# Kernel tuning notes

Hardware: AMD Instinct MI355X
Metric: run time of the kernel (lower is better)

## Reference

```python
import jax, jax.numpy as jnp
import numpy as np

ALPHA = 0.2          # LeakyReLU negative slope
NEG_INF = -9e15      # mask value used by the original module


def setup_inputs() -> dict:
    key = jax.random.key(0)
    k1, k2, k3, k4 = jax.random.split(key, 4)
    N, Din, Dout = 8192, 512, 256
    features = jax.random.normal(k1, (N, Din), dtype=jnp.float32)
    adj = jax.random.randint(k2, (N, N), 0, 2, dtype=jnp.int32)
    W = jax.random.normal(k3, (Din, Dout), dtype=jnp.float32) * (1.414 / np.sqrt(Din))
    a = jax.random.normal(k4, (2 * Dout, 1), dtype=jnp.float32) * (1.414 / np.sqrt(2 * Dout))
    return {"features": features, "adj": adj, "W": W, "a": a}


def reference(features, adj, W, a):
    Dout = W.shape[1]
    Wh = features @ W                       # [N, Dout]
    # e_ij = leakyrelu([Wh_i || Wh_j] @ a) decomposes additively:
    # identical math to the N*N*2D concat in the original, without materializing it.
    src = Wh @ a[:Dout, 0]                  # [N]  contribution of node i
    dst = Wh @ a[Dout:, 0]                  # [N]  contribution of node j
    e = jax.nn.leaky_relu(src[:, None] + dst[None, :], negative_slope=ALPHA)  # [N, N]
    masked = jnp.where(adj > 0, e, NEG_INF)
    attention = jax.nn.softmax(masked, axis=1)   # dropout p=0.0 (eval) -> identity
    h_prime = attention @ Wh                # [N, Dout]
    return jax.nn.elu(h_prime)
```

## Files before the change

kernel.cpp:

```cpp
#include <hip/hip_runtime.h>
#include <hip/hip_bf16.h>

#define NN   8192
#define DIN  512
#define DOUT 256

typedef __attribute__((ext_vector_type(8)))  short s16x8;
typedef __attribute__((ext_vector_type(16))) float f32x16;

static __device__ __forceinline__ unsigned short f2bf(float f) {
    union { float f; unsigned u; } v; v.f = f;
    unsigned r = v.u + 0x7fffu + ((v.u >> 16) & 1u);
    return (unsigned short)(r >> 16);
}

__global__ __launch_bounds__(256) void k_wh2(const float* __restrict__ feat,
                                             const float* __restrict__ W,
                                             const float* __restrict__ a,
                                             unsigned short* __restrict__ WhT,
                                             float* __restrict__ src,
                                             float* __restrict__ dst) {
    __shared__ float lf[16 * DIN];
    __shared__ float red[2][4][16];
    const int tid = threadIdx.x;
    const int i0  = blockIdx.x * 16;
    const int w   = tid >> 6, lane = tid & 63;

    const float4* fsrc = (const float4*)(feat + (size_t)i0 * DIN);
    float4* fdst = (float4*)lf;
    #pragma unroll
    for (int q = 0; q < 8; ++q) fdst[tid + q * 256] = fsrc[tid + q * 256];
    __syncthreads();

    const int c = tid;
    float outs[16];
    #pragma unroll
    for (int r = 0; r < 16; ++r) outs[r] = 0.f;

    for (int k = 0; k < DIN; k += 4) {
        float w0 = W[(k + 0) * DOUT + c];
        float w1 = W[(k + 1) * DOUT + c];
        float w2 = W[(k + 2) * DOUT + c];
        float w3 = W[(k + 3) * DOUT + c];
        #pragma unroll
        for (int r = 0; r < 16; ++r) {
            float4 f = *(const float4*)&lf[r * DIN + k];
            outs[r] = fmaf(f.x, w0, fmaf(f.y, w1, fmaf(f.z, w2, fmaf(f.w, w3, outs[r]))));
        }
    }

    unsigned short tb[16];
    #pragma unroll
    for (int r = 0; r < 16; ++r) tb[r] = f2bf(outs[r]);
    uint4* wt = (uint4*)(WhT + (size_t)c * NN + i0);
    wt[0] = *(uint4*)&tb[0];
    wt[1] = *(uint4*)&tb[8];

    const float as_ = a[c], ad_ = a[DOUT + c];
    #pragma unroll
    for (int r = 0; r < 16; ++r) {
        float s = outs[r] * as_;
        float d = outs[r] * ad_;
        #pragma unroll
        for (int off = 32; off; off >>= 1) {
            s += __shfl_xor(s, off);
            d += __shfl_xor(d, off);
        }
        if (lane == 0) { red[0][w][r] = s; red[1][w][r] = d; }
    }
    __syncthreads();
    if (tid < 16)
        src[i0 + tid] = red[0][0][tid] + red[0][1][tid] + red[0][2][tid] + red[0][3][tid];
    else if (tid < 32) {
        int r = tid - 16;
        dst[i0 + r] = red[1][0][r] + red[1][1][r] + red[1][2][r] + red[1][3][r];
    }
}

__global__ __launch_bounds__(256) void k_mask(const int* __restrict__ adj,
                                              unsigned char* __restrict__ bits) {
    const int row = blockIdx.x;
    const int tid = threadIdx.x;
    const int* base = adj + (size_t)row * NN + tid * 32;
    unsigned int u = 0;
    #pragma unroll
    for (int j = 0; j < 8; ++j) {
        int4 v = *(const int4*)(base + j * 4);
        unsigned int b = (v.x > 0 ? 1u : 0u) | (v.y > 0 ? 2u : 0u) |
                         (v.z > 0 ? 4u : 0u) | (v.w > 0 ? 8u : 0u);
        u |= b << (j * 4);
    }
    *(unsigned int*)(bits + (size_t)row * 1024 + tid * 4) = u;
}


#define STEP6(T, CUR)                                                                    \
{                                                                                        \
        \
    s16x8 bfr_[4];                                                                       \
    _Pragma("unroll")                                                                    \
    for (int ks4 = 0; ks4 < 4; ++ks4)                                                    \
        bfr_[ks4] = *(const s16x8*)(WhTb + (T) * 64 + ks4 * 16);                         \
                                       \
    if ((T) < 31) {                                                                      \
        const unsigned int m8_ = browp[((T) + 1) * 8];                                   \
        float4 d0_ = *(const float4*)(dstp + ((T) + 1) * 64);                            \
        float4 d1_ = *(const float4*)(dstp + ((T) + 1) * 64 + 4);                        \
        const float dd_[8] = {d0_.x, d0_.y, d0_.z, d0_.w, d1_.x, d1_.y, d1_.z, d1_.w};   \
        s16x8 pw_;                                                                       \
        _Pragma("unroll")                                                                \
        for (int jj = 0; jj < 8; ++jj) {                                                 \
            float x_ = si + dd_[jj];                                                     \
            x_ = fmaxf(x_, 0.2f * x_);                               \
            float p_ = (m8_ >> jj) & 1u ? __expf(x_) : 0.f;     \
            den += p_;                                                                   \
            pw_[jj] = (short)f2bf(p_);                                                   \
        }                                                                                \
        *(s16x8*)(Pl[(CUR) ^ 1] + pbyte) = pw_;                                          \
    }                                                                                    \
                             \
    _Pragma("unroll")                                                                    \
    for (int ks4 = 0; ks4 < 4; ++ks4) {                                                  \
        const int kbyte_ = ks4 * 32 + lhi * 16;                                          \
        _Pragma("unroll")                                                                \
        for (int mt = 0; mt < 2; ++mt) {                                                 \
            const int row_ = mt * 32 + l31;                                              \
            s16x8 afv_ = *(const s16x8*)(Pl[CUR] + row_ * 128 +                          \
                                         (kbyte_ ^ ((row_ & 7) << 4)));                  \
            acc[mt] = __builtin_amdgcn_mfma_f32_32x32x16_bf16(afv_, bfr_[ks4], acc[mt], 0, 0, 0); \
        }                                                                                \
    }                                                                                    \
    __syncthreads();                \
}

__global__ __launch_bounds__(512, 4) void k_attn6(const unsigned char* __restrict__ bits,
                                                  const unsigned short* __restrict__ WhT,
                                                  const float* __restrict__ src,
                                                  const float* __restrict__ dstg,
                                                  float* __restrict__ denp,
                                                  float* __restrict__ part) {
    __shared__ __attribute__((aligned(16))) char Pl[2][8192];

    const int tid  = threadIdx.x;
    const int lane = tid & 63;
    const int w    = tid >> 6;
    const int l31  = lane & 31, lhi = lane >> 5;
    const int c0w  = w * 32;

    const int rt  = blockIdx.x & 127;
    const int ks  = blockIdx.x >> 7;
    const int kb0 = ks * 2048;

    const unsigned short* WhTb = WhT + (size_t)(c0w + l31) * NN + kb0 + lhi * 8;

    const int r  = tid >> 3, kb = tid & 7;
    const int gr = rt * 64 + r;
    const float si = src[gr];
    const unsigned char* browp = bits + (size_t)gr * 1024 + ks * 256 + kb;
    const float* dstp = dstg + kb0 + kb * 8;
    const int pbyte = r * 128 + ((kb * 16) ^ ((r & 7) << 4));

    f32x16 acc[2];
    #pragma unroll
    for (int mt = 0; mt < 2; ++mt)
        #pragma unroll
        for (int e = 0; e < 16; ++e) acc[mt][e] = 0.f;
    float den = 0.f;

    {
        const unsigned int m8 = browp[0];
        float4 d0 = *(const float4*)(dstp);
        float4 d1 = *(const float4*)(dstp + 4);
        const float dd[8] = {d0.x, d0.y, d0.z, d0.w, d1.x, d1.y, d1.z, d1.w};
        s16x8 pw;
        #pragma unroll
        for (int jj = 0; jj < 8; ++jj) {
            float x = si + dd[jj];
            x = fmaxf(x, 0.2f * x);
            float p = (m8 >> jj) & 1u ? __expf(x) : 0.f;
            den += p;
            pw[jj] = (short)f2bf(p);
        }
        *(s16x8*)(Pl[0] + pbyte) = pw;
    }
    __syncthreads();

    for (int tt = 0; tt < 16; ++tt) {
        STEP6(2 * tt,     0);
        STEP6(2 * tt + 1, 1);
    }

    den += __shfl_xor(den, 1);
    den += __shfl_xor(den, 2);
    den += __shfl_xor(den, 4);
    if ((tid & 7) == 0) denp[(size_t)ks * NN + gr] = den;

    float* pp = part + (size_t)ks * (NN * DOUT);
    #pragma unroll
    for (int mt = 0; mt < 2; ++mt) {
        #pragma unroll
        for (int e = 0; e < 16; ++e) {
            const int row = rt * 64 + mt * 32 + (e & 3) + 8 * (e >> 2) + 4 * lhi;
            pp[(size_t)row * DOUT + c0w + l31] = acc[mt][e];
        }
    }
}

__global__ __launch_bounds__(256) void k_finish2(const float* __restrict__ part,
                                                 const float* __restrict__ denp,
                                                 float* __restrict__ out) {
    const int idx = blockIdx.x * 256 + threadIdx.x;
    const int row = idx >> 6;
    float den = denp[row] + denp[NN + row] + denp[2 * NN + row] + denp[3 * NN + row];
    float rv = den > 0.f ? 1.f / den : 0.f;
    const int st = NN * DOUT / 4;
    const float4* p = (const float4*)part;
    float4 va = p[idx], vb = p[idx + st], vc = p[idx + 2 * st], vd = p[idx + 3 * st];
    float4 s;
    s.x = (va.x + vb.x + vc.x + vd.x) * rv;
    s.y = (va.y + vb.y + vc.y + vd.y) * rv;
    s.z = (va.z + vb.z + vc.z + vd.z) * rv;
    s.w = (va.w + vb.w + vc.w + vd.w) * rv;
    s.x = s.x > 0.f ? s.x : expm1f(s.x);
    s.y = s.y > 0.f ? s.y : expm1f(s.y);
    s.z = s.z > 0.f ? s.z : expm1f(s.z);
    s.w = s.w > 0.f ? s.w : expm1f(s.w);
    ((float4*)out)[idx] = s;
}

extern "C" void kernel_launch(void* const* d_in, const int* in_sizes, int n_in,
                              void* d_out, int out_size, void* d_ws, size_t ws_size,
                              hipStream_t stream) {
    const float* feat = (const float*)d_in[0];
    const int*   adj  = (const int*)d_in[1];
    const float* W    = (const float*)d_in[2];
    const float* a    = (const float*)d_in[3];
    float* out = (float*)d_out;

    char* ws = (char*)d_ws;
    unsigned short* WhT  = (unsigned short*)ws;
    float*          src  = (float*)(ws + 4194304);
    float*          dst  = (float*)(ws + 4227072);
    float*          denp = (float*)(ws + 4259840);
    unsigned char*  bits = (unsigned char*)(ws + 4390912);
    float*          part = (float*)(ws + 12779520);

    k_mask   <<<8192, 256, 0, stream>>>(adj, bits);
    k_wh2    <<<512,  256, 0, stream>>>(feat, W, a, WhT, src, dst);
    k_attn6  <<<512,  512, 0, stream>>>(bits, WhT, src, dst, denp, part);
    k_finish2<<<2048, 256, 0, stream>>>(part, denp, out);
}
```

Before: 212.1 us.

## Restructure attention kernel: P in registers, WhT via async LDS loads, 8-way K split

The attention kernel is reorganised so each wave owns 32 rows and keeps the computed bf16 probability tile in registers as the MFMA A operand. The full 256-column WhT tile is streamed into double-buffered, swizzled LDS with direct global-to-LDS loads. The K dimension is split 8 ways instead of 4, with 128-row tiles per block, and the finish kernel is widened to sum 8 partials. This removes the LDS round-trip for P and the per-lane global loads of B, and overlaps exp work with MFMA through setprio. The cost is doubled partial-sum traffic, more accumulator registers (8 tiles), and a full vmcnt wait each step.

```diff
diff --git a/kernel.cpp b/kernel.cpp
--- a/kernel.cpp
+++ b/kernel.cpp
@@ -12,6 +12,12 @@
     union { float f; unsigned u; } v; v.f = f;
     unsigned r = v.u + 0x7fffu + ((v.u >> 16) & 1u);
     return (unsigned short)(r >> 16);
+}
+
+static __device__ __forceinline__ void gload_lds16(const void* g, void* l) {
+    __builtin_amdgcn_global_load_lds(
+        (const __attribute__((address_space(1))) unsigned int*)g,
+        (__attribute__((address_space(3))) unsigned int*)l, 16, 0, 0);
 }
 
 __global__ __launch_bounds__(256) void k_wh2(const float* __restrict__ feat,
@@ -93,134 +99,166 @@
     *(unsigned int*)(bits + (size_t)row * 1024 + tid * 4) = u;
 }
 
-
-#define STEP6(T, CUR)                                                                    \
+#define STEP9(T, PA, PB)                                                                 \
 {                                                                                        \
-        \
-    s16x8 bfr_[4];                                                                       \
-    _Pragma("unroll")                                                                    \
-    for (int ks4 = 0; ks4 < 4; ++ks4)                                                    \
-        bfr_[ks4] = *(const s16x8*)(WhTb + (T) * 64 + ks4 * 16);                         \
-                                       \
-    if ((T) < 31) {                                                                      \
-        const unsigned int m8_ = browp[((T) + 1) * 8];                                   \
-        float4 d0_ = *(const float4*)(dstp + ((T) + 1) * 64);                            \
-        float4 d1_ = *(const float4*)(dstp + ((T) + 1) * 64 + 4);                        \
-        const float dd_[8] = {d0_.x, d0_.y, d0_.z, d0_.w, d1_.x, d1_.y, d1_.z, d1_.w};   \
-        s16x8 pw_;                                                                       \
-        _Pragma("unroll")                                                                \
-        for (int jj = 0; jj < 8; ++jj) {                                                 \
-            float x_ = si + dd_[jj];                                                     \
-            x_ = fmaxf(x_, 0.2f * x_);                               \
-            float p_ = (m8_ >> jj) & 1u ? __expf(x_) : 0.f;     \
-            den += p_;                                                                   \
-            pw_[jj] = (short)f2bf(p_);                                                   \
+                    \
+    {                                                                                    \
+        const size_t koff_ = (size_t)(((T) + 1 <= 15) ? (T) + 1 : 15) * 128;             \
+        _Pragma("unroll")                                                                \
+        for (int q = 0; q < 8; ++q)                                                      \
+            gload_lds16(gB + (size_t)q * (32 * NN * 2) + koff_,                          \
+                        Bs[((T) + 1) & 1] + q * 4096 + tid * 16);                        \
+    }                                                                                    \
+                                              \
+    unsigned long long m64_ = 0;                                                         \
+    float4 dv_[8];                                                                       \
+    if ((T) < 15) {                                                                      \
+        m64_ = brow64[(T) + 1];                                                          \
+        _Pragma("unroll")                                                                \
+        for (int ks4 = 0; ks4 < 4; ++ks4) {                                              \
+            dv_[2 * ks4]     = *(const float4*)(dstk + ((T) + 1) * 64 + ks4 * 16 + lhi8);\
+            dv_[2 * ks4 + 1] = *(const float4*)(dstk + ((T) + 1) * 64 + ks4 * 16 + lhi8 + 4);\
         }                                                                                \
-        *(s16x8*)(Pl[(CUR) ^ 1] + pbyte) = pw_;                                          \
-    }                                                                                    \
-                             \
+    }                                                                                    \
+                                                  \
+    __builtin_amdgcn_s_setprio(1);                                                       \
     _Pragma("unroll")                                                                    \
     for (int ks4 = 0; ks4 < 4; ++ks4) {                                                  \
-        const int kbyte_ = ks4 * 32 + lhi * 16;                                          \
-        _Pragma("unroll")                                                                \
-        for (int mt = 0; mt < 2; ++mt) {                                                 \
-            const int row_ = mt * 32 + l31;                                              \
-            s16x8 afv_ = *(const s16x8*)(Pl[CUR] + row_ * 128 +                          \
-                                         (kbyte_ ^ ((row_ & 7) << 4)));                  \
-            acc[mt] = __builtin_amdgcn_mfma_f32_32x32x16_bf16(afv_, bfr_[ks4], acc[mt], 0, 0, 0); \
+        _Pragma("unroll")                                                                \
+        for (int ct = 0; ct < 8; ++ct) {                                                 \
+            const int brow_ = ct * 32 + l31;                                             \
+            s16x8 bfv_ = *(const s16x8*)(Bs[(T) & 1] + brow_ * 128 +                     \
+                                         ((ks4 * 32 + lhi * 16) ^ ((brow_ & 7) << 4)));  \
+            acc[ct] = __builtin_amdgcn_mfma_f32_32x32x16_bf16(PA[ks4], bfv_, acc[ct], 0, 0, 0); \
         }                                                                                \
     }                                                                                    \
-    __syncthreads();                \
-}
-
-__global__ __launch_bounds__(512, 4) void k_attn6(const unsigned char* __restrict__ bits,
+    __builtin_amdgcn_s_setprio(0);                                                       \
+                                 \
+    if ((T) < 15) {                                                                      \
+        const float* df_ = (const float*)dv_;                                            \
+        _Pragma("unroll")                                                                \
+        for (int ks4 = 0; ks4 < 4; ++ks4) {                                              \
+            const unsigned int m8_ = (unsigned int)(m64_ >> (ks4 * 16 + lhi8)) & 0xffu;  \
+            s16x8 pw_;                                                                   \
+            _Pragma("unroll")                                                            \
+            for (int jj = 0; jj < 8; ++jj) {                                             \
+                float x_ = si + df_[ks4 * 8 + jj];                                       \
+                x_ = fmaxf(x_, 0.2f * x_);                           \
+                float p_ = (m8_ >> jj) & 1u ? __expf(x_) : 0.f;      \
+                den += p_;                                                               \
+                pw_[jj] = (short)f2bf(p_);                                               \
+            }                                                                            \
+            PB[ks4] = pw_;                                                               \
+        }                                                                                \
+    }                                                                                    \
+    asm volatile("s_waitcnt vmcnt(0) lgkmcnt(0)" ::: "memory");                          \
+    __builtin_amdgcn_s_barrier();                                                        \
+    __builtin_amdgcn_sched_barrier(0);                                                   \
+}
+
+__global__ __launch_bounds__(256, 2) void k_attn9(const unsigned char* __restrict__ bits,
                                                   const unsigned short* __restrict__ WhT,
                                                   const float* __restrict__ src,
                                                   const float* __restrict__ dstg,
                                                   float* __restrict__ denp,
                                                   float* __restrict__ part) {
-    __shared__ __attribute__((aligned(16))) char Pl[2][8192];
+    __shared__ __attribute__((aligned(16))) char Bs[2][32768];
 
     const int tid  = threadIdx.x;
     const int lane = tid & 63;
-    const int w    = tid >> 6;
+    const int wv   = tid >> 6;
     const int l31  = lane & 31, lhi = lane >> 5;
-    const int c0w  = w * 32;
-
-    const int rt  = blockIdx.x & 127;
-    const int ks  = blockIdx.x >> 7;
-    const int kb0 = ks * 2048;
-
-    const unsigned short* WhTb = WhT + (size_t)(c0w + l31) * NN + kb0 + lhi * 8;
-
-    const int r  = tid >> 3, kb = tid & 7;
-    const int gr = rt * 64 + r;
+    const int lhi8 = lhi * 8;
+
+    const int ks  = blockIdx.x & 7;
+    const int rt  = blockIdx.x >> 3;
+    const int kb0 = ks * 1024;
+
+    const int gr  = rt * 128 + wv * 32 + l31;
     const float si = src[gr];
-    const unsigned char* browp = bits + (size_t)gr * 1024 + ks * 256 + kb;
-    const float* dstp = dstg + kb0 + kb * 8;
-    const int pbyte = r * 128 + ((kb * 16) ^ ((r & 7) << 4));
-
-    f32x16 acc[2];
-    #pragma unroll
-    for (int mt = 0; mt < 2; ++mt)
-        #pragma unroll
-        for (int e = 0; e < 16; ++e) acc[mt][e] = 0.f;
+    const unsigned long long* brow64 =
+        (const unsigned long long*)(bits + (size_t)gr * 1024 + ks * 128);
+    const float* dstk = dstg + kb0;
+
+    const int c0 = tid >> 3;
+    const char* gB = (const char*)WhT + ((size_t)c0 * NN + kb0) * 2
+                   + (((tid & 7) * 16) ^ ((c0 & 7) << 4));
+
+    f32x16 acc[8];
+    #pragma unroll
+    for (int ct = 0; ct < 8; ++ct)
+        #pragma unroll
+        for (int e = 0; e < 16; ++e) acc[ct][e] = 0.f;
     float den = 0.f;
 
+    s16x8 pA[4], pB[4];
+
+    #pragma unroll
+    for (int q = 0; q < 8; ++q)
+        gload_lds16(gB + (size_t)q * (32 * NN * 2), Bs[0] + q * 4096 + tid * 16);
     {
-        const unsigned int m8 = browp[0];
-        float4 d0 = *(const float4*)(dstp);
-        float4 d1 = *(const float4*)(dstp + 4);
-        const float dd[8] = {d0.x, d0.y, d0.z, d0.w, d1.x, d1.y, d1.z, d1.w};
-        s16x8 pw;
-        #pragma unroll
-        for (int jj = 0; jj < 8; ++jj) {
-            float x = si + dd[jj];
-            x = fmaxf(x, 0.2f * x);
-            float p = (m8 >> jj) & 1u ? __expf(x) : 0.f;
-            den += p;
-            pw[jj] = (short)f2bf(p);
-        }
-        *(s16x8*)(Pl[0] + pbyte) = pw;
-    }
-    __syncthreads();
-
-    for (int tt = 0; tt < 16; ++tt) {
-        STEP6(2 * tt,     0);
-        STEP6(2 * tt + 1, 1);
-    }
-
-    den += __shfl_xor(den, 1);
-    den += __shfl_xor(den, 2);
-    den += __shfl_xor(den, 4);
-    if ((tid & 7) == 0) denp[(size_t)ks * NN + gr] = den;
+        const unsigned long long m64 = brow64[0];
+        #pragma unroll
+        for (int ks4 = 0; ks4 < 4; ++ks4) {
+            float4 d0 = *(const float4*)(dstk + ks4 * 16 + lhi8);
+            float4 d1 = *(const float4*)(dstk + ks4 * 16 + lhi8 + 4);
+            const float df[8] = {d0.x, d0.y, d0.z, d0.w, d1.x, d1.y, d1.z, d1.w};
+            const unsigned int m8 = (unsigned int)(m64 >> (ks4 * 16 + lhi8)) & 0xffu;
+            s16x8 pw;
+            #pragma unroll
+            for (int jj = 0; jj < 8; ++jj) {
+                float x = si + df[jj];
+                x = fmaxf(x, 0.2f * x);
+                float p = (m8 >> jj) & 1u ? __expf(x) : 0.f;
+                den += p;
+                pw[jj] = (short)f2bf(p);
+            }
+            pA[ks4] = pw;
+        }
+    }
+    asm volatile("s_waitcnt vmcnt(0) lgkmcnt(0)" ::: "memory");
+    __builtin_amdgcn_s_barrier();
+    __builtin_amdgcn_sched_barrier(0);
+
+    #pragma unroll
+    for (int tt = 0; tt < 8; ++tt) {
+        STEP9(2 * tt,     pA, pB);
+        STEP9(2 * tt + 1, pB, pA);
+    }
+
+    den += __shfl_xor(den, 32);
+    if (lhi == 0) denp[(size_t)ks * NN + gr] = den;
 
     float* pp = part + (size_t)ks * (NN * DOUT);
     #pragma unroll
-    for (int mt = 0; mt < 2; ++mt) {
+    for (int ct = 0; ct < 8; ++ct) {
         #pragma unroll
         for (int e = 0; e < 16; ++e) {
-            const int row = rt * 64 + mt * 32 + (e & 3) + 8 * (e >> 2) + 4 * lhi;
-            pp[(size_t)row * DOUT + c0w + l31] = acc[mt][e];
-        }
-    }
-}
-
-__global__ __launch_bounds__(256) void k_finish2(const float* __restrict__ part,
+            const int row = rt * 128 + wv * 32 + (e & 3) + 8 * (e >> 2) + 4 * lhi;
+            pp[(size_t)row * DOUT + ct * 32 + l31] = acc[ct][e];
+        }
+    }
+}
+
+__global__ __launch_bounds__(256) void k_finish3(const float* __restrict__ part,
                                                  const float* __restrict__ denp,
                                                  float* __restrict__ out) {
     const int idx = blockIdx.x * 256 + threadIdx.x;
     const int row = idx >> 6;
-    float den = denp[row] + denp[NN + row] + denp[2 * NN + row] + denp[3 * NN + row];
+    float den = 0.f;
+    #pragma unroll
+    for (int i = 0; i < 8; ++i) den += denp[(size_t)i * NN + row];
     float rv = den > 0.f ? 1.f / den : 0.f;
-    const int st = NN * DOUT / 4;
+    const size_t st = (size_t)NN * DOUT / 4;
     const float4* p = (const float4*)part;
-    float4 va = p[idx], vb = p[idx + st], vc = p[idx + 2 * st], vd = p[idx + 3 * st];
+    float sx = 0.f, sy = 0.f, sz = 0.f, sw = 0.f;
+    #pragma unroll
+    for (int i = 0; i < 8; ++i) {
+        float4 v = p[idx + i * st];
+        sx += v.x; sy += v.y; sz += v.z; sw += v.w;
+    }
     float4 s;
-    s.x = (va.x + vb.x + vc.x + vd.x) * rv;
-    s.y = (va.y + vb.y + vc.y + vd.y) * rv;
-    s.z = (va.z + vb.z + vc.z + vd.z) * rv;
-    s.w = (va.w + vb.w + vc.w + vd.w) * rv;
+    s.x = sx * rv; s.y = sy * rv; s.z = sz * rv; s.w = sw * rv;
     s.x = s.x > 0.f ? s.x : expm1f(s.x);
     s.y = s.y > 0.f ? s.y : expm1f(s.y);
     s.z = s.z > 0.f ? s.z : expm1f(s.z);
@@ -242,11 +280,11 @@
     float*          src  = (float*)(ws + 4194304);
     float*          dst  = (float*)(ws + 4227072);
     float*          denp = (float*)(ws + 4259840);
-    unsigned char*  bits = (unsigned char*)(ws + 4390912);
-    float*          part = (float*)(ws + 12779520);
+    unsigned char*  bits = (unsigned char*)(ws + 4521984);
+    float*          part = (float*)(ws + 12910592);
 
     k_mask   <<<8192, 256, 0, stream>>>(adj, bits);
     k_wh2    <<<512,  256, 0, stream>>>(feat, W, a, WhT, src, dst);
-    k_attn6  <<<512,  512, 0, stream>>>(bits, WhT, src, dst, denp, part);
-    k_finish2<<<2048, 256, 0, stream>>>(part, denp, out);
-}
+    k_attn9  <<<512,  256, 0, stream>>>(bits, WhT, src, dst, denp, part);
+    k_finish3<<<2048, 256, 0, stream>>>(part, denp, out);
+}
```

Result: no change. 211.4 us (-0.3%).
